# Performance work log

Measured on AMD Instinct MI355X. Metric: run time of the kernel, lower is better.

## Reference

```python
import jax, jax.numpy as jnp
import numpy as np

BN_EPS = 1e-3  # keras BatchNormalization default epsilon


def setup_inputs() -> dict:
    key = jax.random.key(0)
    k1, k2, k3 = jax.random.split(key, 3)
    B, H, W, C, K = 16, 32, 32, 256, 32
    support = 1.0 / (K * C) ** 0.5
    inputs = jax.random.normal(k1, (B, H, W, C), dtype=jnp.float32)
    codewords = jax.random.uniform(k2, (1, 1, K, C), minval=-support, maxval=support, dtype=jnp.float32)
    smoothing_factors = jax.random.uniform(k3, (1, 1, K), minval=-1.0, maxval=0.0, dtype=jnp.float32)
    gamma = jnp.ones((C,), dtype=jnp.float32)
    beta = jnp.zeros((C,), dtype=jnp.float32)
    return {"inputs": inputs, "codewords": codewords, "smoothing_factors": smoothing_factors,
            "gamma": gamma, "beta": beta}


def reference(inputs, codewords, smoothing_factors, gamma, beta):
    B, H, W, C = inputs.shape
    n = H * W
    feats = inputs.reshape(B, n, 1, C)
    # residuals: [B, n, K, C]
    residuals = feats - codewords
    # squared norms over features -> [B, n, K]
    sqnorms = jnp.sum(residuals * residuals, axis=-1)
    # smoothed softmax over codewords
    w = jax.nn.softmax(sqnorms * smoothing_factors, axis=-1)  # [B, n, K]
    # softmax-weighted residual sum over spatial positions -> [B, K, C]
    enc = jnp.einsum('bnk,bnkc->bkc', w, residuals)
    # BatchNorm over last axis (training-mode batch stats over axes (0,1))
    mean = jnp.mean(enc, axis=(0, 1))
    var = jnp.var(enc, axis=(0, 1))
    bn = (enc - mean) * jax.lax.rsqrt(var + BN_EPS) * gamma + beta
    # ReLU then sum over codewords -> [B, C]
    return jnp.sum(jax.nn.relu(bn), axis=1)
```

## Files before the change

### kernel.cpp

```cpp
#include <hip/hip_runtime.h>
#include <hip/hip_bf16.h>


#define BN_EPS 1e-3f

typedef __attribute__((ext_vector_type(8))) short short8;
typedef __attribute__((ext_vector_type(4))) float f32x4;

static __device__ inline unsigned short f2bf(float f) {
    unsigned int u = __float_as_uint(f);
    unsigned int r = (u + 0x7fffu + ((u >> 16) & 1u)) >> 16;
    return (unsigned short)r;
}

static __device__ inline short8 pack8(float4 u, float4 v) {
    short8 r;
    r[0] = (short)f2bf(u.x); r[1] = (short)f2bf(u.y);
    r[2] = (short)f2bf(u.z); r[3] = (short)f2bf(u.w);
    r[4] = (short)f2bf(v.x); r[5] = (short)f2bf(v.y);
    r[6] = (short)f2bf(v.z); r[7] = (short)f2bf(v.w);
    return r;
}

#if __has_builtin(__builtin_amdgcn_global_load_lds)
#define HAVE_GLOAD_LDS 1
typedef const __attribute__((address_space(1))) void* as1_cvp;
typedef __attribute__((address_space(3))) void* as3_vp;
static __device__ inline void gload_lds16(const void* g, void* s) {
    __builtin_amdgcn_global_load_lds((as1_cvp)g, (as3_vp)s, 16, 0, 0);
}
#else
#define HAVE_GLOAD_LDS 0
#endif

union P01 {
    struct {
        unsigned short cwbf[32][264];
        float ccred[8][32];
    } p0;
    struct {
        float4 dred[2][2][2][64];
        float  xxr[2][2][16];
    } p1;
};

__global__ __launch_bounds__(256, 2) void enc_main_mfma(
    const float* __restrict__ x, const float* __restrict__ cw,
    const float* __restrict__ sf, float* __restrict__ pS1, float* __restrict__ pW)
{
    const int bid = blockIdx.x;
    const int b   = bid >> 5;
    const int jb  = bid & 31;
    const int t = threadIdx.x;
    const int w = t >> 6;
    const int lane = t & 63;

    __shared__ float4 xs4[32][65];
    __shared__ unsigned short xbf[32][264];
    __shared__ P01 u;
    __shared__ unsigned short wT[32][40];
    __shared__ float  cc_lds[32];
    __shared__ float  sf_lds[32];
    __shared__ float  w_lds[32][33];

    const int nbase = jb * 32;
    const float4* gx4 = (const float4*)(x + (size_t)b * 1024 * 256) + (size_t)nbase * 64;
#if HAVE_GLOAD_LDS
    #pragma unroll
    for (int i = 0; i < 8; ++i) {
        const int row = w * 8 + i;
        gload_lds16(gx4 + row * 64 + lane, &xs4[row][0]);
    }
#else
    {
        const int p = t >> 3, q = t & 7;
        #pragma unroll
        for (int j = 0; j < 8; ++j)
            xs4[p][q + 8 * j] = gx4[p * 64 + q + 8 * j];
    }
#endif
    {
        const int k = t >> 3, seg = t & 7;
        const float4* cw4 = (const float4*)cw;
        float s = 0.f;
        #pragma unroll
        for (int jj = 0; jj < 4; ++jj) {
            float4 u0 = cw4[k * 64 + seg * 8 + 2 * jj];
            float4 u1 = cw4[k * 64 + seg * 8 + 2 * jj + 1];
            s += u0.x * u0.x + u0.y * u0.y + u0.z * u0.z + u0.w * u0.w
               + u1.x * u1.x + u1.y * u1.y + u1.z * u1.z + u1.w * u1.w;
            *(short8*)&u.p0.cwbf[k][seg * 32 + 8 * jj] = pack8(u0, u1);
        }
        u.p0.ccred[seg][k] = s;
    }
    if (t < 32) sf_lds[t] = sf[t];
    __syncthreads();

    const int mt = w >> 1, half = w & 1;
    const int lrow = lane & 15;
    const int g = lane >> 4;
    const float* xsf = (const float*)xs4;

    f32x4 D0 = {0.f, 0.f, 0.f, 0.f}, D1 = {0.f, 0.f, 0.f, 0.f};
    float xxp = 0.f;
    #pragma unroll
    for (int ks = 0; ks < 4; ++ks) {
        const int ch = half * 128 + ks * 32 + g * 8;
        const int row = mt * 16 + lrow;
        const float* ap = xsf + row * 260 + ch;
        float4 uu = *(const float4*)ap;
        float4 vv = *(const float4*)(ap + 4);
        xxp += uu.x * uu.x + uu.y * uu.y + uu.z * uu.z + uu.w * uu.w
             + vv.x * vv.x + vv.y * vv.y + vv.z * vv.z + vv.w * vv.w;
        short8 a = pack8(uu, vv);
        *(short8*)&xbf[row][ch] = a;
        short8 b0 = *(const short8*)&u.p0.cwbf[lrow][ch];
        short8 b1 = *(const short8*)&u.p0.cwbf[16 + lrow][ch];
        D0 = __builtin_amdgcn_mfma_f32_16x16x32_bf16(a, b0, D0, 0, 0, 0);
        D1 = __builtin_amdgcn_mfma_f32_16x16x32_bf16(a, b1, D1, 0, 0, 0);
    }
    xxp += __shfl_xor(xxp, 16, 64);
    xxp += __shfl_xor(xxp, 32, 64);
    if (t < 32) {
        float s = 0.f;
        #pragma unroll
        for (int j = 0; j < 8; ++j) s += u.p0.ccred[j][t];
        cc_lds[t] = s;
    }
    __syncthreads();

    if (lane < 16) u.p1.xxr[mt][half][lane] = xxp;
    u.p1.dred[mt][half][0][lane] = make_float4(D0[0], D0[1], D0[2], D0[3]);
    u.p1.dred[mt][half][1][lane] = make_float4(D1[0], D1[1], D1[2], D1[3]);
    __syncthreads();

    {
        float4 a0 = u.p1.dred[mt][0][0][lane], b0 = u.p1.dred[mt][1][0][lane];
        float4 a1 = u.p1.dred[mt][0][1][lane], b1 = u.p1.dred[mt][1][1][lane];
        float d0[4] = {a0.x + b0.x, a0.y + b0.y, a0.z + b0.z, a0.w + b0.w};
        float d1[4] = {a1.x + b1.x, a1.y + b1.y, a1.z + b1.z, a1.w + b1.w};
        const int k0 = lane & 15, k1 = 16 + k0;
        const float sf0 = sf_lds[k0], sf1 = sf_lds[k1];
        const float cc0 = cc_lds[k0], cc1 = cc_lds[k1];
        #pragma unroll
        for (int r = 0; r < 4; ++r) {
            const int pl = (lane >> 4) * 4 + r;
            const float xxv = u.p1.xxr[mt][0][pl] + u.p1.xxr[mt][1][pl];
            float s0 = sf0 * (xxv - 2.f * d0[r] + cc0);
            float s1 = sf1 * (xxv - 2.f * d1[r] + cc1);
            float m = fmaxf(s0, s1);
            #pragma unroll
            for (int msk = 1; msk <= 8; msk <<= 1) m = fmaxf(m, __shfl_xor(m, msk, 64));
            float e0 = __expf(s0 - m), e1 = __expf(s1 - m);
            float sm = e0 + e1;
            #pragma unroll
            for (int msk = 1; msk <= 8; msk <<= 1) sm += __shfl_xor(sm, msk, 64);
            const float inv = 1.f / sm;
            if (half == 0) {
                const int n = mt * 16 + pl;
                const float w0 = e0 * inv, w1 = e1 * inv;
                w_lds[n][k0] = w0;
                w_lds[n][k1] = w1;
                wT[k0][n] = f2bf(w0);
                wT[k1][n] = f2bf(w1);
            }
        }
    }
    __syncthreads();

    {
        short8 a0 = *(const short8*)&wT[lrow][8 * g];
        short8 a1 = *(const short8*)&wT[16 + lrow][8 * g];
        f32x4 E00 = {0,0,0,0}, E01 = {0,0,0,0}, E02 = {0,0,0,0}, E03 = {0,0,0,0};
        f32x4 E10 = {0,0,0,0}, E11 = {0,0,0,0}, E12 = {0,0,0,0}, E13 = {0,0,0,0};
        const int cbase = w * 64;
        const unsigned short* xbu = &xbf[0][0];
        #pragma unroll
        for (int nt = 0; nt < 4; ++nt) {
            const int c = cbase + nt * 16 + lrow;
            short8 bf;
            #pragma unroll
            for (int e = 0; e < 8; ++e)
                bf[e] = (short)xbu[(8 * g + e) * 264 + c];
            if (nt == 0) { E00 = __builtin_amdgcn_mfma_f32_16x16x32_bf16(a0, bf, E00, 0,0,0);
                           E10 = __builtin_amdgcn_mfma_f32_16x16x32_bf16(a1, bf, E10, 0,0,0); }
            if (nt == 1) { E01 = __builtin_amdgcn_mfma_f32_16x16x32_bf16(a0, bf, E01, 0,0,0);
                           E11 = __builtin_amdgcn_mfma_f32_16x16x32_bf16(a1, bf, E11, 0,0,0); }
            if (nt == 2) { E02 = __builtin_amdgcn_mfma_f32_16x16x32_bf16(a0, bf, E02, 0,0,0);
                           E12 = __builtin_amdgcn_mfma_f32_16x16x32_bf16(a1, bf, E12, 0,0,0); }
            if (nt == 3) { E03 = __builtin_amdgcn_mfma_f32_16x16x32_bf16(a0, bf, E03, 0,0,0);
                           E13 = __builtin_amdgcn_mfma_f32_16x16x32_bf16(a1, bf, E13, 0,0,0); }
        }
        float* dst = pS1 + (size_t)bid * 8192;
        const int krow = 4 * g;
        #pragma unroll
        for (int reg = 0; reg < 4; ++reg) {
            const int k0r = (krow + reg) * 256;
            const int k1r = (16 + krow + reg) * 256;
            dst[k0r + cbase +  0 + lrow] = E00[reg];
            dst[k0r + cbase + 16 + lrow] = E01[reg];
            dst[k0r + cbase + 32 + lrow] = E02[reg];
            dst[k0r + cbase + 48 + lrow] = E03[reg];
            dst[k1r + cbase +  0 + lrow] = E10[reg];
            dst[k1r + cbase + 16 + lrow] = E11[reg];
            dst[k1r + cbase + 32 + lrow] = E12[reg];
            dst[k1r + cbase + 48 + lrow] = E13[reg];
        }
    }
    if (t < 32) {
        float s = 0.f;
        #pragma unroll
        for (int p = 0; p < 32; ++p) s += w_lds[p][t];
        pW[bid * 32 + t] = s;
    }
}

__global__ __launch_bounds__(256) void enc_reduce(
    const float* __restrict__ pS1, const float* __restrict__ pW,
    const float* __restrict__ cw, float* __restrict__ enc)
{
    const int row = blockIdx.x;
    const int b = row >> 5;
    const int k = row & 31;
    const int c = threadIdx.x;
    float s = 0.f;
    #pragma unroll
    for (int jj = 0; jj < 32; ++jj)
        s += pS1[(size_t)(b * 32 + jj) * 8192 + k * 256 + c];
    const int lane = c & 63;
    float wp = pW[(b * 32 + (lane & 31)) * 32 + k];
    #pragma unroll
    for (int m = 1; m <= 16; m <<= 1) wp += __shfl_xor(wp, m, 64);
    enc[row * 256 + c] = s - wp * cw[k * 256 + c];
}

__global__ __launch_bounds__(256) void enc_stats2(
    const float* __restrict__ enc, float* __restrict__ pst)
{
    const int p = blockIdx.x;
    const int c = threadIdx.x;
    float s = 0.f, ss = 0.f;
    #pragma unroll
    for (int r = 0; r < 16; ++r) {
        float v = enc[(p * 16 + r) * 256 + c];
        s += v;
        ss = fmaf(v, v, ss);
    }
    pst[p * 512 + c] = s;
    pst[p * 512 + 256 + c] = ss;
}

__global__ __launch_bounds__(256) void enc_out(
    const float* __restrict__ enc, const float* __restrict__ pst,
    const float* __restrict__ gamma, const float* __restrict__ beta,
    float* __restrict__ out)
{
    const int b = blockIdx.x;
    const int c = threadIdx.x;
    float S = 0.f, SS = 0.f;
    #pragma unroll
    for (int p = 0; p < 32; ++p) {
        S  += pst[p * 512 + c];
        SS += pst[p * 512 + 256 + c];
    }
    const float mean = S * (1.f / 512.f);
    const float var = SS * (1.f / 512.f) - mean * mean;
    const float g = gamma[c] * rsqrtf(var + BN_EPS);
    const float bt = beta[c];
    float o = 0.f;
    #pragma unroll
    for (int k = 0; k < 32; ++k) {
        float e = enc[(b * 32 + k) * 256 + c];
        float v = (e - mean) * g + bt;
        o += fmaxf(v, 0.f);
    }
    out[b * 256 + c] = o;
}

extern "C" void kernel_launch(void* const* d_in, const int* in_sizes, int n_in,
                              void* d_out, int out_size, void* d_ws, size_t ws_size,
                              hipStream_t stream) {
    const float* x     = (const float*)d_in[0];
    const float* cw    = (const float*)d_in[1];
    const float* sf    = (const float*)d_in[2];
    const float* gamma = (const float*)d_in[3];
    const float* beta  = (const float*)d_in[4];
    float* out = (float*)d_out;
    float* ws  = (float*)d_ws;

    float* pS1 = ws;
    float* pW  = pS1 + (size_t)512 * 8192;
    float* enc = pW + (size_t)512 * 32;
    float* pst = enc + (size_t)512 * 256;

    enc_main_mfma<<<512, 256, 0, stream>>>(x, cw, sf, pS1, pW);
    enc_reduce<<<512, 256, 0, stream>>>(pS1, pW, cw, enc);
    enc_stats2<<<32, 256, 0, stream>>>(enc, pst);
    enc_out<<<16, 256, 0, stream>>>(enc, pst, gamma, beta, out);
}
```

Measured before the change: 29.04 us.

## Process 64 positions per 512-thread block with double tile loop and prefetch

Each main-kernel block now handles 64 spatial positions in two 32-row tiles with 512 threads (8 waves). The second tile's load is issued into LDS while the first tile's softmax runs, and the encoding accumulators stay in registers across both tiles. This halves the partial-sum buffer that the reduce kernel must read. In exchange there are fewer blocks (256) and one block per CU, which reduces parallelism. The reduce and stats kernels are adjusted to the new partial counts.

```diff
diff --git a/kernel.cpp b/kernel.cpp
--- a/kernel.cpp
+++ b/kernel.cpp
@@ -33,184 +33,204 @@
 #define HAVE_GLOAD_LDS 0
 #endif
 
-union P01 {
-    struct {
-        unsigned short cwbf[32][264];
-        float ccred[8][32];
-    } p0;
-    struct {
-        float4 dred[2][2][2][64];
-        float  xxr[2][2][16];
-    } p1;
-};
-
-__global__ __launch_bounds__(256, 2) void enc_main_mfma(
+__global__ __launch_bounds__(512, 1) void enc_main_mfma(
     const float* __restrict__ x, const float* __restrict__ cw,
     const float* __restrict__ sf, float* __restrict__ pS1, float* __restrict__ pW)
 {
     const int bid = blockIdx.x;
-    const int b   = bid >> 5;
-    const int jb  = bid & 31;
+    const int b   = bid >> 4;
+    const int jb2 = bid & 15;
     const int t = threadIdx.x;
     const int w = t >> 6;
     const int lane = t & 63;
+    const int mt   = w >> 2;
+    const int half = (w >> 1) & 1;
+    const int dup  = w & 1;
+    const int lrow = lane & 15;
+    const int g    = lane >> 4;
 
     __shared__ float4 xs4[32][65];
+    __shared__ unsigned short cwbf[32][264];
+    __shared__ float  ccred[16][32];
+    __shared__ float4 dred[2][2][2][2][64];
+    __shared__ float  xxr[2][2][2][16];
     __shared__ unsigned short xbf[32][264];
-    __shared__ P01 u;
     __shared__ unsigned short wT[32][40];
+    __shared__ float  w_lds[2][32][33];
     __shared__ float  cc_lds[32];
     __shared__ float  sf_lds[32];
-    __shared__ float  w_lds[32][33];
-
-    const int nbase = jb * 32;
-    const float4* gx4 = (const float4*)(x + (size_t)b * 1024 * 256) + (size_t)nbase * 64;
+
+    const float4* gx4 = (const float4*)(x + (size_t)b * 1024 * 256)
+                        + (size_t)jb2 * 64 * 64;
+
 #if HAVE_GLOAD_LDS
     #pragma unroll
-    for (int i = 0; i < 8; ++i) {
-        const int row = w * 8 + i;
+    for (int i = 0; i < 4; ++i) {
+        const int row = w * 4 + i;
         gload_lds16(gx4 + row * 64 + lane, &xs4[row][0]);
     }
 #else
     {
-        const int p = t >> 3, q = t & 7;
-        #pragma unroll
-        for (int j = 0; j < 8; ++j)
-            xs4[p][q + 8 * j] = gx4[p * 64 + q + 8 * j];
+        const int p = t >> 4, q = t & 15;
+        #pragma unroll
+        for (int j = 0; j < 4; ++j)
+            xs4[p][q + 16 * j] = gx4[p * 64 + q + 16 * j];
     }
 #endif
     {
-        const int k = t >> 3, seg = t & 7;
+        const int k = t >> 4, seg = t & 15;
         const float4* cw4 = (const float4*)cw;
         float s = 0.f;
         #pragma unroll
-        for (int jj = 0; jj < 4; ++jj) {
-            float4 u0 = cw4[k * 64 + seg * 8 + 2 * jj];
-            float4 u1 = cw4[k * 64 + seg * 8 + 2 * jj + 1];
+        for (int jj = 0; jj < 2; ++jj) {
+            float4 u0 = cw4[k * 64 + seg * 4 + 2 * jj];
+            float4 u1 = cw4[k * 64 + seg * 4 + 2 * jj + 1];
             s += u0.x * u0.x + u0.y * u0.y + u0.z * u0.z + u0.w * u0.w
                + u1.x * u1.x + u1.y * u1.y + u1.z * u1.z + u1.w * u1.w;
-            *(short8*)&u.p0.cwbf[k][seg * 32 + 8 * jj] = pack8(u0, u1);
-        }
-        u.p0.ccred[seg][k] = s;
+            *(short8*)&cwbf[k][seg * 16 + 8 * jj] = pack8(u0, u1);
+        }
+        ccred[seg][k] = s;
     }
     if (t < 32) sf_lds[t] = sf[t];
     __syncthreads();
 
-    const int mt = w >> 1, half = w & 1;
-    const int lrow = lane & 15;
-    const int g = lane >> 4;
-    const float* xsf = (const float*)xs4;
-
-    f32x4 D0 = {0.f, 0.f, 0.f, 0.f}, D1 = {0.f, 0.f, 0.f, 0.f};
-    float xxp = 0.f;
-    #pragma unroll
-    for (int ks = 0; ks < 4; ++ks) {
-        const int ch = half * 128 + ks * 32 + g * 8;
-        const int row = mt * 16 + lrow;
-        const float* ap = xsf + row * 260 + ch;
-        float4 uu = *(const float4*)ap;
-        float4 vv = *(const float4*)(ap + 4);
-        xxp += uu.x * uu.x + uu.y * uu.y + uu.z * uu.z + uu.w * uu.w
-             + vv.x * vv.x + vv.y * vv.y + vv.z * vv.z + vv.w * vv.w;
-        short8 a = pack8(uu, vv);
-        *(short8*)&xbf[row][ch] = a;
-        short8 b0 = *(const short8*)&u.p0.cwbf[lrow][ch];
-        short8 b1 = *(const short8*)&u.p0.cwbf[16 + lrow][ch];
-        D0 = __builtin_amdgcn_mfma_f32_16x16x32_bf16(a, b0, D0, 0, 0, 0);
-        D1 = __builtin_amdgcn_mfma_f32_16x16x32_bf16(a, b1, D1, 0, 0, 0);
-    }
-    xxp += __shfl_xor(xxp, 16, 64);
-    xxp += __shfl_xor(xxp, 32, 64);
     if (t < 32) {
         float s = 0.f;
         #pragma unroll
-        for (int j = 0; j < 8; ++j) s += u.p0.ccred[j][t];
+        for (int j = 0; j < 16; ++j) s += ccred[j][t];
         cc_lds[t] = s;
     }
-    __syncthreads();
-
-    if (lane < 16) u.p1.xxr[mt][half][lane] = xxp;
-    u.p1.dred[mt][half][0][lane] = make_float4(D0[0], D0[1], D0[2], D0[3]);
-    u.p1.dred[mt][half][1][lane] = make_float4(D1[0], D1[1], D1[2], D1[3]);
-    __syncthreads();
-
-    {
-        float4 a0 = u.p1.dred[mt][0][0][lane], b0 = u.p1.dred[mt][1][0][lane];
-        float4 a1 = u.p1.dred[mt][0][1][lane], b1 = u.p1.dred[mt][1][1][lane];
-        float d0[4] = {a0.x + b0.x, a0.y + b0.y, a0.z + b0.z, a0.w + b0.w};
-        float d1[4] = {a1.x + b1.x, a1.y + b1.y, a1.z + b1.z, a1.w + b1.w};
-        const int k0 = lane & 15, k1 = 16 + k0;
-        const float sf0 = sf_lds[k0], sf1 = sf_lds[k1];
-        const float cc0 = cc_lds[k0], cc1 = cc_lds[k1];
-        #pragma unroll
-        for (int r = 0; r < 4; ++r) {
-            const int pl = (lane >> 4) * 4 + r;
-            const float xxv = u.p1.xxr[mt][0][pl] + u.p1.xxr[mt][1][pl];
-            float s0 = sf0 * (xxv - 2.f * d0[r] + cc0);
-            float s1 = sf1 * (xxv - 2.f * d1[r] + cc1);
-            float m = fmaxf(s0, s1);
-            #pragma unroll
-            for (int msk = 1; msk <= 8; msk <<= 1) m = fmaxf(m, __shfl_xor(m, msk, 64));
-            float e0 = __expf(s0 - m), e1 = __expf(s1 - m);
-            float sm = e0 + e1;
-            #pragma unroll
-            for (int msk = 1; msk <= 8; msk <<= 1) sm += __shfl_xor(sm, msk, 64);
-            const float inv = 1.f / sm;
-            if (half == 0) {
-                const int n = mt * 16 + pl;
-                const float w0 = e0 * inv, w1 = e1 * inv;
-                w_lds[n][k0] = w0;
-                w_lds[n][k1] = w1;
-                wT[k0][n] = f2bf(w0);
-                wT[k1][n] = f2bf(w1);
+
+    f32x4 E00 = {0,0,0,0}, E01 = {0,0,0,0}, E10 = {0,0,0,0}, E11 = {0,0,0,0};
+    const float* xsf = (const float*)xs4;
+
+    #pragma unroll
+    for (int tile = 0; tile < 2; ++tile) {
+        f32x4 D0 = {0,0,0,0}, D1 = {0,0,0,0};
+        float xxp = 0.f;
+        #pragma unroll
+        for (int k2 = 0; k2 < 2; ++k2) {
+            const int ks = dup * 2 + k2;
+            const int ch = half * 128 + ks * 32 + g * 8;
+            const int row = mt * 16 + lrow;
+            const float* ap = xsf + row * 260 + ch;
+            float4 uu = *(const float4*)ap;
+            float4 vv = *(const float4*)(ap + 4);
+            xxp += uu.x * uu.x + uu.y * uu.y + uu.z * uu.z + uu.w * uu.w
+                 + vv.x * vv.x + vv.y * vv.y + vv.z * vv.z + vv.w * vv.w;
+            short8 a = pack8(uu, vv);
+            *(short8*)&xbf[row][ch] = a;
+            short8 b0 = *(const short8*)&cwbf[lrow][ch];
+            short8 b1 = *(const short8*)&cwbf[16 + lrow][ch];
+            D0 = __builtin_amdgcn_mfma_f32_16x16x32_bf16(a, b0, D0, 0, 0, 0);
+            D1 = __builtin_amdgcn_mfma_f32_16x16x32_bf16(a, b1, D1, 0, 0, 0);
+        }
+        xxp += __shfl_xor(xxp, 16, 64);
+        xxp += __shfl_xor(xxp, 32, 64);
+        if (lane < 16) xxr[mt][half][dup][lane] = xxp;
+        dred[mt][half][dup][0][lane] = make_float4(D0[0], D0[1], D0[2], D0[3]);
+        dred[mt][half][dup][1][lane] = make_float4(D1[0], D1[1], D1[2], D1[3]);
+        __syncthreads();
+
+        if (tile == 0) {
+#if HAVE_GLOAD_LDS
+            #pragma unroll
+            for (int i = 0; i < 4; ++i) {
+                const int row = w * 4 + i;
+                gload_lds16(gx4 + (32 + row) * 64 + lane, &xs4[row][0]);
             }
-        }
-    }
-    __syncthreads();
-
-    {
-        short8 a0 = *(const short8*)&wT[lrow][8 * g];
-        short8 a1 = *(const short8*)&wT[16 + lrow][8 * g];
-        f32x4 E00 = {0,0,0,0}, E01 = {0,0,0,0}, E02 = {0,0,0,0}, E03 = {0,0,0,0};
-        f32x4 E10 = {0,0,0,0}, E11 = {0,0,0,0}, E12 = {0,0,0,0}, E13 = {0,0,0,0};
-        const int cbase = w * 64;
-        const unsigned short* xbu = &xbf[0][0];
-        #pragma unroll
-        for (int nt = 0; nt < 4; ++nt) {
-            const int c = cbase + nt * 16 + lrow;
-            short8 bf;
-            #pragma unroll
-            for (int e = 0; e < 8; ++e)
-                bf[e] = (short)xbu[(8 * g + e) * 264 + c];
-            if (nt == 0) { E00 = __builtin_amdgcn_mfma_f32_16x16x32_bf16(a0, bf, E00, 0,0,0);
-                           E10 = __builtin_amdgcn_mfma_f32_16x16x32_bf16(a1, bf, E10, 0,0,0); }
-            if (nt == 1) { E01 = __builtin_amdgcn_mfma_f32_16x16x32_bf16(a0, bf, E01, 0,0,0);
-                           E11 = __builtin_amdgcn_mfma_f32_16x16x32_bf16(a1, bf, E11, 0,0,0); }
-            if (nt == 2) { E02 = __builtin_amdgcn_mfma_f32_16x16x32_bf16(a0, bf, E02, 0,0,0);
-                           E12 = __builtin_amdgcn_mfma_f32_16x16x32_bf16(a1, bf, E12, 0,0,0); }
-            if (nt == 3) { E03 = __builtin_amdgcn_mfma_f32_16x16x32_bf16(a0, bf, E03, 0,0,0);
-                           E13 = __builtin_amdgcn_mfma_f32_16x16x32_bf16(a1, bf, E13, 0,0,0); }
-        }
-        float* dst = pS1 + (size_t)bid * 8192;
-        const int krow = 4 * g;
-        #pragma unroll
-        for (int reg = 0; reg < 4; ++reg) {
-            const int k0r = (krow + reg) * 256;
-            const int k1r = (16 + krow + reg) * 256;
-            dst[k0r + cbase +  0 + lrow] = E00[reg];
-            dst[k0r + cbase + 16 + lrow] = E01[reg];
-            dst[k0r + cbase + 32 + lrow] = E02[reg];
-            dst[k0r + cbase + 48 + lrow] = E03[reg];
-            dst[k1r + cbase +  0 + lrow] = E10[reg];
-            dst[k1r + cbase + 16 + lrow] = E11[reg];
-            dst[k1r + cbase + 32 + lrow] = E12[reg];
-            dst[k1r + cbase + 48 + lrow] = E13[reg];
-        }
+#else
+            const int p = t >> 4, q = t & 15;
+            #pragma unroll
+            for (int j = 0; j < 4; ++j)
+                xs4[p][q + 16 * j] = gx4[(32 + p) * 64 + q + 16 * j];
+#endif
+        }
+
+        {
+            const int k0 = lrow, k1 = 16 + lrow;
+            float d0[4], d1[4];
+            #pragma unroll
+            for (int nt = 0; nt < 2; ++nt) {
+                float4 s00 = dred[mt][0][0][nt][lane];
+                float4 s01 = dred[mt][0][1][nt][lane];
+                float4 s10 = dred[mt][1][0][nt][lane];
+                float4 s11 = dred[mt][1][1][nt][lane];
+                float* dd = nt ? d1 : d0;
+                dd[0] = s00.x + s01.x + s10.x + s11.x;
+                dd[1] = s00.y + s01.y + s10.y + s11.y;
+                dd[2] = s00.z + s01.z + s10.z + s11.z;
+                dd[3] = s00.w + s01.w + s10.w + s11.w;
+            }
+            const float sf0 = sf_lds[k0], sf1 = sf_lds[k1];
+            const float cc0 = cc_lds[k0], cc1 = cc_lds[k1];
+            #pragma unroll
+            for (int r = 0; r < 4; ++r) {
+                const int pl = g * 4 + r;
+                const float xxv = xxr[mt][0][0][pl] + xxr[mt][0][1][pl]
+                                + xxr[mt][1][0][pl] + xxr[mt][1][1][pl];
+                float s0 = sf0 * (xxv - 2.f * d0[r] + cc0);
+                float s1 = sf1 * (xxv - 2.f * d1[r] + cc1);
+                float m = fmaxf(s0, s1);
+                #pragma unroll
+                for (int msk = 1; msk <= 8; msk <<= 1) m = fmaxf(m, __shfl_xor(m, msk, 64));
+                float e0 = __expf(s0 - m), e1 = __expf(s1 - m);
+                float sm = e0 + e1;
+                #pragma unroll
+                for (int msk = 1; msk <= 8; msk <<= 1) sm += __shfl_xor(sm, msk, 64);
+                const float inv = 1.f / sm;
+                if (half == 0 && dup == 0) {
+                    const int n = mt * 16 + pl;
+                    const float w0v = e0 * inv, w1v = e1 * inv;
+                    w_lds[tile][n][k0] = w0v;
+                    w_lds[tile][n][k1] = w1v;
+                    wT[k0][n] = f2bf(w0v);
+                    wT[k1][n] = f2bf(w1v);
+                }
+            }
+        }
+        asm volatile("s_waitcnt lgkmcnt(0)" ::: "memory");
+        __builtin_amdgcn_sched_barrier(0);
+        __builtin_amdgcn_s_barrier();
+        __builtin_amdgcn_sched_barrier(0);
+
+        {
+            short8 a0 = *(const short8*)&wT[lrow][8 * g];
+            short8 a1 = *(const short8*)&wT[16 + lrow][8 * g];
+            const unsigned short* xbu = &xbf[0][0];
+            #pragma unroll
+            for (int nt = 0; nt < 2; ++nt) {
+                const int c = w * 32 + nt * 16 + lrow;
+                short8 bf;
+                #pragma unroll
+                for (int e = 0; e < 8; ++e)
+                    bf[e] = (short)xbu[(8 * g + e) * 264 + c];
+                if (nt == 0) {
+                    E00 = __builtin_amdgcn_mfma_f32_16x16x32_bf16(a0, bf, E00, 0, 0, 0);
+                    E10 = __builtin_amdgcn_mfma_f32_16x16x32_bf16(a1, bf, E10, 0, 0, 0);
+                } else {
+                    E01 = __builtin_amdgcn_mfma_f32_16x16x32_bf16(a0, bf, E01, 0, 0, 0);
+                    E11 = __builtin_amdgcn_mfma_f32_16x16x32_bf16(a1, bf, E11, 0, 0, 0);
+                }
+            }
+        }
+        if (tile == 0) __syncthreads();
+    }
+
+    float* dst = pS1 + (size_t)bid * 8192;
+    #pragma unroll
+    for (int reg = 0; reg < 4; ++reg) {
+        const int k0r = (4 * g + reg) * 256;
+        const int k1r = (16 + 4 * g + reg) * 256;
+        dst[k0r + w * 32 +  0 + lrow] = E00[reg];
+        dst[k0r + w * 32 + 16 + lrow] = E01[reg];
+        dst[k1r + w * 32 +  0 + lrow] = E10[reg];
+        dst[k1r + w * 32 + 16 + lrow] = E11[reg];
     }
     if (t < 32) {
         float s = 0.f;
         #pragma unroll
-        for (int p = 0; p < 32; ++p) s += w_lds[p][t];
+        for (int p = 0; p < 32; ++p) s += w_lds[0][p][t] + w_lds[1][p][t];
         pW[bid * 32 + t] = s;
     }
 }
@@ -225,12 +245,12 @@
     const int c = threadIdx.x;
     float s = 0.f;
     #pragma unroll
-    for (int jj = 0; jj < 32; ++jj)
-        s += pS1[(size_t)(b * 32 + jj) * 8192 + k * 256 + c];
+    for (int jj = 0; jj < 16; ++jj)
+        s += pS1[(size_t)(b * 16 + jj) * 8192 + k * 256 + c];
     const int lane = c & 63;
-    float wp = pW[(b * 32 + (lane & 31)) * 32 + k];
-    #pragma unroll
-    for (int m = 1; m <= 16; m <<= 1) wp += __shfl_xor(wp, m, 64);
+    float wp = pW[(b * 16 + (lane & 15)) * 32 + k];
+    #pragma unroll
+    for (int m = 1; m <= 8; m <<= 1) wp += __shfl_xor(wp, m, 64);
     enc[row * 256 + c] = s - wp * cw[k * 256 + c];
 }
 
@@ -241,8 +261,8 @@
     const int c = threadIdx.x;
     float s = 0.f, ss = 0.f;
     #pragma unroll
-    for (int r = 0; r < 16; ++r) {
-        float v = enc[(p * 16 + r) * 256 + c];
+    for (int r = 0; r < 8; ++r) {
+        float v = enc[(p * 8 + r) * 256 + c];
         s += v;
         ss = fmaf(v, v, ss);
     }
@@ -258,8 +278,8 @@
     const int b = blockIdx.x;
     const int c = threadIdx.x;
     float S = 0.f, SS = 0.f;
-    #pragma unroll
-    for (int p = 0; p < 32; ++p) {
+    #pragma unroll 8
+    for (int p = 0; p < 64; ++p) {
         S  += pst[p * 512 + c];
         SS += pst[p * 512 + 256 + c];
     }
@@ -289,12 +309,12 @@
     float* ws  = (float*)d_ws;
 
     float* pS1 = ws;
-    float* pW  = pS1 + (size_t)512 * 8192;
-    float* enc = pW + (size_t)512 * 32;
+    float* pW  = pS1 + (size_t)256 * 8192;
+    float* enc = pW + (size_t)256 * 32;
     float* pst = enc + (size_t)512 * 256;
 
-    enc_main_mfma<<<512, 256, 0, stream>>>(x, cw, sf, pS1, pW);
+    enc_main_mfma<<<256, 512, 0, stream>>>(x, cw, sf, pS1, pW);
     enc_reduce<<<512, 256, 0, stream>>>(pS1, pW, cw, enc);
-    enc_stats2<<<32, 256, 0, stream>>>(enc, pst);
+    enc_stats2<<<64, 256, 0, stream>>>(enc, pst);
     enc_out<<<16, 256, 0, stream>>>(enc, pst, gamma, beta, out);
 }
```

Measured after the change: 26.66 us. -8.2%, faster.
